# Kernel optimization log

Measured on AMD Instinct MI355X. Metric: run time of the kernel, lower is better.

The kernel has to match this reference:

```python
import jax, jax.numpy as jnp
import numpy as np

N, T, S, B, E, H = 2, 1024, 1024, 4, 1024, 16
HD = E // H

def setup_inputs() -> dict:
    key = jax.random.key(0)
    ks = jax.random.split(key, 12)
    s = E ** -0.5
    return {
        "query": jax.random.normal(ks[0], (T, B, E), jnp.float32),
        "keys": jax.random.normal(ks[1], (N, S, B, E), jnp.float32),
        "masks": jax.random.randint(ks[2], (N, B, S), 0, 2) == 1,
        "Wq": jax.random.normal(ks[3], (N, E, E), jnp.float32) * s,
        "bq": jax.random.normal(ks[4], (N, E), jnp.float32) * 0.02,
        "Wk": jax.random.normal(ks[5], (N, E, E), jnp.float32) * s,
        "bk": jax.random.normal(ks[6], (N, E), jnp.float32) * 0.02,
        "Wv": jax.random.normal(ks[7], (N, E, E), jnp.float32) * s,
        "bv": jax.random.normal(ks[8], (N, E), jnp.float32) * 0.02,
        "Wo": jax.random.normal(ks[9], (E, E), jnp.float32) * s,
        "bo": jax.random.normal(ks[10], (E,), jnp.float32) * 0.02,
    }


def reference(query, keys, masks, Wq, bq, Wk, bk, Wv, bv, Wo, bo):
    # query: [T,B,E]; keys: [N,S,B,E]; masks: [N,B,S] (True = padded)
    scaling = HD ** -0.5
    # Per-source linear projections (torch Linear: x @ W.T + b)
    q = (jnp.einsum('tbe,nfe->ntbf', query, Wq) + bq[:, None, None, :]) * scaling
    k = jnp.einsum('nsbe,nfe->nsbf', keys, Wk) + bk[:, None, None, :]
    v = jnp.einsum('nsbe,nfe->nsbf', keys, Wv) + bv[:, None, None, :]
    # split heads -> [n,b,h,len,hd]
    q = q.reshape(N, T, B, H, HD).transpose(0, 2, 3, 1, 4)
    k = k.reshape(N, S, B, H, HD).transpose(0, 2, 3, 1, 4)
    v = v.reshape(N, S, B, H, HD).transpose(0, 2, 3, 1, 4)
    # per-source masked scores: [n,b,h,t,s]
    scores = jnp.einsum('nbhtd,nbhsd->nbhts', q, k)
    scores = jnp.where(masks[:, :, None, None, :], -jnp.inf, scores)
    # concat sources along key axis (source-major, matching torch.cat order)
    scores = scores.transpose(1, 2, 3, 0, 4).reshape(B, H, T, N * S)
    probs = jax.nn.softmax(scores, axis=-1)
    v_cat = v.transpose(1, 2, 0, 3, 4).reshape(B, H, N * S, HD)
    out = jnp.einsum('bhtk,bhkd->bhtd', probs, v_cat)  # [B,H,T,HD]
    out = out.transpose(2, 0, 1, 3).reshape(T, B, E)
    return out @ Wo.T + bo
```

## Files before the change

kernel.cpp:

```cpp
#include <hip/hip_runtime.h>


typedef __bf16 bf16x8 __attribute__((ext_vector_type(8)));
typedef unsigned short u16x8 __attribute__((ext_vector_type(8)));
typedef unsigned short u16x4 __attribute__((ext_vector_type(4)));
typedef float f32x4 __attribute__((ext_vector_type(4)));

#define OFF_QP 0ul
#define OFF_KP (8ul << 20)
#define OFF_VP (16ul << 20)
#define OFF_AO (24ul << 20)
#define OFF_XQ (28ul << 20)
#define OFF_XK (32ul << 20)
#define OFF_W (40ul << 20)
#define OFF_WO (46ul << 20)

__device__ __forceinline__ unsigned short f2bf(float x) {
  unsigned u = __builtin_bit_cast(unsigned, x);
  return (unsigned short)((u + 0x7fffu + ((u >> 16) & 1u)) >> 16);
}
__device__ __forceinline__ float bf2f(unsigned short h) {
  return __builtin_bit_cast(float, (unsigned)h << 16);
}
__device__ __forceinline__ void gload16(const void* g, void* l) {
  __builtin_amdgcn_global_load_lds(
      (const __attribute__((address_space(1))) unsigned*)g,
      (__attribute__((address_space(3))) unsigned*)l, 16, 0, 0);
}

__global__ __launch_bounds__(256) void cvt_all(
    const float* __restrict__ q, const float* __restrict__ k,
    const float* __restrict__ wq, const float* __restrict__ wk,
    const float* __restrict__ wv, const float* __restrict__ wo,
    unsigned short* __restrict__ ws) {
  const int z = blockIdx.y;
  const float* src;
  unsigned short* dst;
  unsigned nq;
  if (z == 0)      { src = q;  dst = ws + OFF_XQ;              nq = 1u << 20; }
  else if (z == 1) { src = k;  dst = ws + OFF_XK;              nq = 2u << 20; }
  else if (z == 2) { src = wq; dst = ws + OFF_W;               nq = 1u << 19; }
  else if (z == 3) { src = wk; dst = ws + OFF_W + (2ul << 20); nq = 1u << 19; }
  else if (z == 4) { src = wv; dst = ws + OFF_W + (4ul << 20); nq = 1u << 19; }
  else             { src = wo; dst = ws + OFF_WO;              nq = 1u << 18; }
  for (unsigned i = blockIdx.x * 256 + threadIdx.x; i < nq; i += gridDim.x * 256) {
    float4 v = ((const float4*)src)[i];
    u16x4 o = {f2bf(v.x), f2bf(v.y), f2bf(v.z), f2bf(v.w)};
    *(u16x4*)&dst[(size_t)i * 4] = o;
  }
}

__device__ __forceinline__ void gemm_mfma(const unsigned short* __restrict__ A,
                                          const unsigned short* __restrict__ B,
                                          const float* __restrict__ bias,
                                          void* __restrict__ outp, int nsrc,
                                          float scale, int mode) {
  __shared__ unsigned short As[4096];
  __shared__ unsigned short Bs[4096];
  const int tid = threadIdx.x;
  const int w = tid >> 6, lane = tid & 63;
  const int wr = w >> 1, wc = w & 1;
  const long row0 = (long)blockIdx.x * 128, col0 = (long)blockIdx.y * 128;

  f32x4 acc[4][4] = {};

  const unsigned short* ga0 = A + (row0 + lane) * 1024 + w * 8;
  const unsigned short* ga1 = ga0 + 64 * 1024;
  const unsigned short* gb0 = B + (col0 + lane) * 1024 + w * 8;
  const unsigned short* gb1 = gb0 + 64 * 1024;
  unsigned short* la0 = &As[w * 1024];
  unsigned short* la1 = la0 + 512;
  unsigned short* lb0 = &Bs[w * 1024];
  unsigned short* lb1 = lb0 + 512;

  const int kb = (lane >> 4) * 1024;
  const int fr = lane & 15;

  for (int k0 = 0; k0 < 1024; k0 += 32) {
    gload16(ga0 + k0, la0);
    gload16(ga1 + k0, la1);
    gload16(gb0 + k0, lb0);
    gload16(gb1 + k0, lb1);
    __syncthreads();
    bf16x8 af[4], bfr[4];
#pragma unroll
    for (int m = 0; m < 4; ++m)
      af[m] = __builtin_bit_cast(
          bf16x8, *(const u16x8*)&As[kb + (wr * 64 + m * 16 + fr) * 8]);
#pragma unroll
    for (int nn = 0; nn < 4; ++nn)
      bfr[nn] = __builtin_bit_cast(
          bf16x8, *(const u16x8*)&Bs[kb + (wc * 64 + nn * 16 + fr) * 8]);
#pragma unroll
    for (int m = 0; m < 4; ++m)
#pragma unroll
      for (int nn = 0; nn < 4; ++nn)
        acc[m][nn] = __builtin_amdgcn_mfma_f32_16x16x32_bf16(af[m], bfr[nn],
                                                             acc[m][nn], 0, 0, 0);
    __syncthreads();
  }

  const int fq = lane >> 4;
#pragma unroll
  for (int m = 0; m < 4; ++m)
#pragma unroll
    for (int nn = 0; nn < 4; ++nn) {
      const long col = col0 + wc * 64 + nn * 16 + fr;
      const float bcol = bias[col];
#pragma unroll
      for (int r = 0; r < 4; ++r) {
        const long row = row0 + wr * 64 + m * 16 + fq * 4 + r;
        const float v = (acc[m][nn][r] + bcol) * scale;
        const long t = row >> 2, bb = row & 3;
        const long h = col >> 6, d = col & 63;
        const long nbh = ((long)nsrc * 4 + bb) * 16 + h;
        if (mode == 2)
          ((float*)outp)[row * 1024 + col] = v;
        else if (mode == 0)
          ((unsigned short*)outp)[(nbh * 1024 + t) * 64 + d] = f2bf(v);
        else
          ((unsigned short*)outp)[nbh * 65536 + d * 1024 + t] = f2bf(v);
      }
    }
}

__global__ __launch_bounds__(256) void proj_fused(unsigned short* __restrict__ ws,
                                                  const float* __restrict__ bq,
                                                  const float* __restrict__ bk,
                                                  const float* __restrict__ bv) {
  const int z = blockIdx.z;
  const int n = z & 1, type = z >> 1;
  const unsigned short* A =
      ws + (type == 0 ? OFF_XQ : OFF_XK + (unsigned long)n * (4ul << 20));
  const unsigned short* B = ws + OFF_W + (unsigned long)(type * 2 + n) * (1ul << 20);
  const float* bias = ((type == 0) ? bq : (type == 1) ? bk : bv) + n * 1024;
  unsigned short* out = ws + (type == 0 ? OFF_QP : (type == 1) ? OFF_KP : OFF_VP);
  const float scale = (type == 0) ? 0.125f : 1.0f;
  gemm_mfma(A, B, bias, out, n, scale, (type == 2) ? 1 : 0);
}

__global__ __launch_bounds__(256) void gemm_out(const unsigned short* __restrict__ ws_c,
                                                const float* __restrict__ bias,
                                                float* __restrict__ out) {
  gemm_mfma(ws_c + OFF_AO, ws_c + OFF_WO, bias, (void*)out, 0, 1.0f, 2);
}

__global__ __launch_bounds__(256) void attn_mfma(
    const unsigned short* __restrict__ qp, const unsigned short* __restrict__ kp,
    const unsigned short* __restrict__ vpt, const int* __restrict__ masks,
    unsigned short* __restrict__ ao) {
  __shared__ __align__(16) unsigned short Ks[64 * 72];
  __shared__ __align__(16) unsigned short Vt[64 * 72];
  __shared__ __align__(16) unsigned short Pl[4 * 16 * 72];
  __shared__ __align__(16) float mba[2 * 1024];

  const int tid = threadIdx.x;
  const int w = tid >> 6, l = tid & 63;
  const int g = l >> 4, q16 = l & 15;
  const int b = blockIdx.z, h = blockIdx.y;
  const int t0 = blockIdx.x * 64 + w * 16;

#pragma unroll
  for (int p = 0; p < 2; ++p) {
    const int idx = tid + p * 256;
    const int n = idx >> 8, off = (idx & 255) * 4;
    const int4 mi = *(const int4*)&masks[((long)n * 4 + b) * 1024 + off];
    f32x4 mf = {mi.x ? -3.0e38f : 0.0f, mi.y ? -3.0e38f : 0.0f,
                mi.z ? -3.0e38f : 0.0f, mi.w ? -3.0e38f : 0.0f};
    *(f32x4*)&mba[n * 1024 + off] = mf;
  }

  float m = -3.0e38f, ls = 0.0f;
  f32x4 o[4] = {};

  unsigned short* pw = &Pl[(w * 16 + q16) * 72];

  for (int n = 0; n < 2; ++n) {
    const long nbh = ((long)n * 4 + b) * 16 + h;
    const unsigned short* qrp = qp + (nbh * 1024 + t0 + q16) * 64 + g * 8;
    const bf16x8 qf0 = __builtin_bit_cast(bf16x8, *(const u16x8*)&qrp[0]);
    const bf16x8 qf1 = __builtin_bit_cast(bf16x8, *(const u16x8*)&qrp[32]);
    const unsigned short* kbase = kp + nbh * 65536;
    const unsigned short* vbase = vpt + nbh * 65536;
    const float* mb = &mba[n * 1024];

    for (int s0 = 0; s0 < 1024; s0 += 64) {
      __syncthreads();
#pragma unroll
      for (int p = 0; p < 2; ++p) {
        const int id = tid + p * 256;
        const int r8 = id >> 3, c8 = (id & 7) * 8;
        *(u16x8*)&Ks[r8 * 72 + c8] = *(const u16x8*)&kbase[(long)(s0 + r8) * 64 + c8];
        *(u16x8*)&Vt[r8 * 72 + c8] = *(const u16x8*)&vbase[(long)r8 * 1024 + s0 + c8];
      }
      __syncthreads();

      f32x4 st[4] = {};
#pragma unroll
      for (int kf = 0; kf < 4; ++kf) {
        const bf16x8 ka0 = __builtin_bit_cast(
            bf16x8, *(const u16x8*)&Ks[(kf * 16 + q16) * 72 + g * 8]);
        const bf16x8 ka1 = __builtin_bit_cast(
            bf16x8, *(const u16x8*)&Ks[(kf * 16 + q16) * 72 + 32 + g * 8]);
        st[kf] = __builtin_amdgcn_mfma_f32_16x16x32_bf16(ka0, qf0, st[kf], 0, 0, 0);
        st[kf] = __builtin_amdgcn_mfma_f32_16x16x32_bf16(ka1, qf1, st[kf], 0, 0, 0);
      }
      float mt = -3.0e38f;
#pragma unroll
      for (int kf = 0; kf < 4; ++kf) {
        const f32x4 mv = *(const f32x4*)&mb[s0 + kf * 16 + g * 4];
#pragma unroll
        for (int r = 0; r < 4; ++r) {
          st[kf][r] += mv[r];
          mt = fmaxf(mt, st[kf][r]);
        }
      }
      mt = fmaxf(mt, __shfl_xor(mt, 16, 64));
      mt = fmaxf(mt, __shfl_xor(mt, 32, 64));
      const float mnew = fmaxf(m, mt);
      const float corr = __expf(m - mnew);
      float ps = 0.0f;
#pragma unroll
      for (int kf = 0; kf < 4; ++kf)
#pragma unroll
        for (int r = 0; r < 4; ++r) {
          st[kf][r] = __expf(st[kf][r] - mnew);
          ps += st[kf][r];
        }
      ps += __shfl_xor(ps, 16, 64);
      ps += __shfl_xor(ps, 32, 64);
      ls = ls * corr + ps;
      m = mnew;
#pragma unroll
      for (int df = 0; df < 4; ++df)
#pragma unroll
        for (int r = 0; r < 4; ++r) o[df][r] *= corr;
#pragma unroll
      for (int kf = 0; kf < 4; ++kf) {
        u16x4 pp = {f2bf(st[kf][0]), f2bf(st[kf][1]), f2bf(st[kf][2]),
                    f2bf(st[kf][3])};
        *(u16x4*)&pw[kf * 16 + g * 4] = pp;
      }
      const bf16x8 pb0 = __builtin_bit_cast(bf16x8, *(const u16x8*)&pw[g * 8]);
      const bf16x8 pb1 = __builtin_bit_cast(bf16x8, *(const u16x8*)&pw[32 + g * 8]);
#pragma unroll
      for (int df = 0; df < 4; ++df) {
        const bf16x8 va0 = __builtin_bit_cast(
            bf16x8, *(const u16x8*)&Vt[(df * 16 + q16) * 72 + g * 8]);
        const bf16x8 va1 = __builtin_bit_cast(
            bf16x8, *(const u16x8*)&Vt[(df * 16 + q16) * 72 + 32 + g * 8]);
        o[df] = __builtin_amdgcn_mfma_f32_16x16x32_bf16(va0, pb0, o[df], 0, 0, 0);
        o[df] = __builtin_amdgcn_mfma_f32_16x16x32_bf16(va1, pb1, o[df], 0, 0, 0);
      }
    }
  }

  const float inv = 1.0f / ls;
  unsigned short* orow = ao + ((long)(t0 + q16) * 4 + b) * 1024 + h * 64 + g * 4;
#pragma unroll
  for (int df = 0; df < 4; ++df) {
    u16x4 ov = {f2bf(o[df][0] * inv), f2bf(o[df][1] * inv),
                f2bf(o[df][2] * inv), f2bf(o[df][3] * inv)};
    *(u16x4*)&orow[df * 16] = ov;
  }
}

extern "C" void kernel_launch(void* const* d_in, const int* in_sizes, int n_in,
                              void* d_out, int out_size, void* d_ws, size_t ws_size,
                              hipStream_t stream) {
  const float* query = (const float*)d_in[0];
  const float* keys = (const float*)d_in[1];
  const int* masks = (const int*)d_in[2];
  const float* bq = (const float*)d_in[4];
  const float* bk = (const float*)d_in[6];
  const float* bv = (const float*)d_in[8];
  const float* bo = (const float*)d_in[10];

  unsigned short* ws = (unsigned short*)d_ws;
  const dim3 blk(256);

  cvt_all<<<dim3(512, 6), blk, 0, stream>>>(query, keys, (const float*)d_in[3],
                                            (const float*)d_in[5],
                                            (const float*)d_in[7],
                                            (const float*)d_in[9], ws);
  proj_fused<<<dim3(32, 8, 6), blk, 0, stream>>>(ws, bq, bk, bv);
  attn_mfma<<<dim3(16, 16, 4), blk, 0, stream>>>(
      ws + OFF_QP, ws + OFF_KP, ws + OFF_VP, masks, ws + OFF_AO);
  gemm_out<<<dim3(32, 8, 1), blk, 0, stream>>>(ws, bo, (float*)d_out);
}
```

Baseline: 361.2 us.

## Double-buffer GEMM LDS tiles and register-prefetch K/V tiles in attention

```diff
diff --git a/kernel.cpp b/kernel.cpp
--- a/kernel.cpp
+++ b/kernel.cpp
@@ -55,8 +55,8 @@
                                           const float* __restrict__ bias,
                                           void* __restrict__ outp, int nsrc,
                                           float scale, int mode) {
-  __shared__ unsigned short As[4096];
-  __shared__ unsigned short Bs[4096];
+  __shared__ unsigned short As[2][4096];
+  __shared__ unsigned short Bs[2][4096];
   const int tid = threadIdx.x;
   const int w = tid >> 6, lane = tid & 63;
   const int wr = w >> 1, wc = w & 1;
@@ -68,29 +68,32 @@
   const unsigned short* ga1 = ga0 + 64 * 1024;
   const unsigned short* gb0 = B + (col0 + lane) * 1024 + w * 8;
   const unsigned short* gb1 = gb0 + 64 * 1024;
-  unsigned short* la0 = &As[w * 1024];
-  unsigned short* la1 = la0 + 512;
-  unsigned short* lb0 = &Bs[w * 1024];
-  unsigned short* lb1 = lb0 + 512;
 
   const int kb = (lane >> 4) * 1024;
   const int fr = lane & 15;
 
+  auto stage = [&](int buf, int k0) {
+    gload16(ga0 + k0, &As[buf][w * 1024]);
+    gload16(ga1 + k0, &As[buf][w * 1024 + 512]);
+    gload16(gb0 + k0, &Bs[buf][w * 1024]);
+    gload16(gb1 + k0, &Bs[buf][w * 1024 + 512]);
+  };
+
+  stage(0, 0);
+  __syncthreads();
+
   for (int k0 = 0; k0 < 1024; k0 += 32) {
-    gload16(ga0 + k0, la0);
-    gload16(ga1 + k0, la1);
-    gload16(gb0 + k0, lb0);
-    gload16(gb1 + k0, lb1);
-    __syncthreads();
+    const int cur = (k0 >> 5) & 1;
+    if (k0 + 32 < 1024) stage(cur ^ 1, k0 + 32);
     bf16x8 af[4], bfr[4];
 #pragma unroll
     for (int m = 0; m < 4; ++m)
       af[m] = __builtin_bit_cast(
-          bf16x8, *(const u16x8*)&As[kb + (wr * 64 + m * 16 + fr) * 8]);
+          bf16x8, *(const u16x8*)&As[cur][kb + (wr * 64 + m * 16 + fr) * 8]);
 #pragma unroll
     for (int nn = 0; nn < 4; ++nn)
       bfr[nn] = __builtin_bit_cast(
-          bf16x8, *(const u16x8*)&Bs[kb + (wc * 64 + nn * 16 + fr) * 8]);
+          bf16x8, *(const u16x8*)&Bs[cur][kb + (wc * 64 + nn * 16 + fr) * 8]);
 #pragma unroll
     for (int m = 0; m < 4; ++m)
 #pragma unroll
@@ -175,25 +178,36 @@
 
   unsigned short* pw = &Pl[(w * 16 + q16) * 72];
 
+  const int r8 = tid >> 3, c8 = (tid & 7) * 8;
+  u16x8 pkA, pkB, pvA, pvB;
+  auto pfetch = [&](int tt) {
+    const int nn = tt >> 4, ss = (tt & 15) << 6;
+    const long nbh2 = ((long)nn * 4 + b) * 16 + h;
+    const unsigned short* kb2 = kp + nbh2 * 65536;
+    const unsigned short* vb2 = vpt + nbh2 * 65536;
+    pkA = *(const u16x8*)&kb2[(long)(ss + r8) * 64 + c8];
+    pkB = *(const u16x8*)&kb2[(long)(ss + r8 + 32) * 64 + c8];
+    pvA = *(const u16x8*)&vb2[(long)r8 * 1024 + ss + c8];
+    pvB = *(const u16x8*)&vb2[(long)(r8 + 32) * 1024 + ss + c8];
+  };
+  pfetch(0);
+  int tt = 0;
+
   for (int n = 0; n < 2; ++n) {
     const long nbh = ((long)n * 4 + b) * 16 + h;
     const unsigned short* qrp = qp + (nbh * 1024 + t0 + q16) * 64 + g * 8;
     const bf16x8 qf0 = __builtin_bit_cast(bf16x8, *(const u16x8*)&qrp[0]);
     const bf16x8 qf1 = __builtin_bit_cast(bf16x8, *(const u16x8*)&qrp[32]);
-    const unsigned short* kbase = kp + nbh * 65536;
-    const unsigned short* vbase = vpt + nbh * 65536;
     const float* mb = &mba[n * 1024];
 
     for (int s0 = 0; s0 < 1024; s0 += 64) {
       __syncthreads();
-#pragma unroll
-      for (int p = 0; p < 2; ++p) {
-        const int id = tid + p * 256;
-        const int r8 = id >> 3, c8 = (id & 7) * 8;
-        *(u16x8*)&Ks[r8 * 72 + c8] = *(const u16x8*)&kbase[(long)(s0 + r8) * 64 + c8];
-        *(u16x8*)&Vt[r8 * 72 + c8] = *(const u16x8*)&vbase[(long)r8 * 1024 + s0 + c8];
-      }
+      *(u16x8*)&Ks[r8 * 72 + c8] = pkA;
+      *(u16x8*)&Ks[(r8 + 32) * 72 + c8] = pkB;
+      *(u16x8*)&Vt[r8 * 72 + c8] = pvA;
+      *(u16x8*)&Vt[(r8 + 32) * 72 + c8] = pvB;
       __syncthreads();
+      if (tt + 1 < 32) pfetch(tt + 1);
 
       f32x4 st[4] = {};
 #pragma unroll
@@ -252,6 +266,7 @@
         o[df] = __builtin_amdgcn_mfma_f32_16x16x32_bf16(va0, pb0, o[df], 0, 0, 0);
         o[df] = __builtin_amdgcn_mfma_f32_16x16x32_bf16(va1, pb1, o[df], 0, 0, 0);
       }
+      ++tt;
     }
   }
 
```

New measurement: 356.5 us. No clear change (-1.3%).
